# Performance work log

Hardware: AMD Instinct MI355X
Metric: run time of the kernel (lower is better)

## Reference

```python
import jax, jax.numpy as jnp
import numpy as np

B, S, D = 2, 2048, 1024
H = 16
HD = D // H

def setup_inputs() -> dict:
    key = jax.random.key(0)
    ks = jax.random.split(key, 6)
    sc = 0.02
    return {
        'x': jax.random.normal(ks[0], (B, S, D), jnp.float32),
        'Wq': jax.random.normal(ks[1], (D, D), jnp.float32) * sc,
        'Wk': jax.random.normal(ks[2], (D, D), jnp.float32) * sc,
        'Wv': jax.random.normal(ks[3], (D, D), jnp.float32) * sc,
        'Wo': jax.random.normal(ks[4], (D, D), jnp.float32) * sc,
        'bo': jnp.zeros((D,), jnp.float32),
    }

def reference(x, Wq, Wk, Wv, Wo, bo):
    b, s, d_in = x.shape
    # torch Linear: y = x @ W.T
    q = jnp.einsum('bsd,ed->bse', x, Wq)
    k = jnp.einsum('bsd,ed->bse', x, Wk)
    v = jnp.einsum('bsd,ed->bse', x, Wv)
    # [b, h, s, hd]
    q = q.reshape(b, s, H, HD).transpose(0, 2, 1, 3)
    k = k.reshape(b, s, H, HD).transpose(0, 2, 1, 3)
    v = v.reshape(b, s, H, HD).transpose(0, 2, 1, 3)
    # NOTE: original divides by sqrt(d_out), not sqrt(head_dim)
    scores = jnp.einsum('bhqd,bhkd->bhqk', q, k) / jnp.sqrt(jnp.float32(D))
    causal = jnp.tril(jnp.ones((s, s), dtype=bool))  # True = keep
    scores = jnp.where(causal[None, None], scores, -jnp.inf)
    attn = jax.nn.softmax(scores, axis=-1)
    ctx = jnp.einsum('bhqk,bhkd->bhqd', attn, v)
    ctx = ctx.transpose(0, 2, 1, 3).reshape(b, s, D)
    return jnp.einsum('bsd,ed->bse', ctx, Wo) + bo
```

## Files before the change

### kernel.cpp

```cpp
#include <hip/hip_runtime.h>
#include <hip/hip_bf16.h>
#include <stdint.h>

typedef unsigned short u16;
typedef __attribute__((ext_vector_type(8))) short short8;
typedef __attribute__((ext_vector_type(4))) float f32x4;
typedef __attribute__((ext_vector_type(16))) float f32x16;
typedef __attribute__((ext_vector_type(4))) u16 u16x4;

#define NB 2
#define NS 2048
#define ND 1024
#define NH 16
#define NM 4096

#define QSCALE 0.045084220f

#if __has_builtin(__builtin_amdgcn_exp2f)
#define EXP2(x) __builtin_amdgcn_exp2f(x)
#else
__device__ __forceinline__ float __exp2_asm(float x){
  float r;
  asm("v_exp_f32 %0, %1" : "=v"(r) : "v"(x));
  return r;
}
#define EXP2(x) __exp2_asm(x)
#endif
#if __has_builtin(__builtin_amdgcn_rcpf)
#define RCP(x) __builtin_amdgcn_rcpf(x)
#else
#define RCP(x) (1.0f / (x))
#endif

__device__ __forceinline__ u16 f2bf(float f){
  union { float f; unsigned u; } v; v.f = f;
  unsigned r = v.u + 0x7fff + ((v.u >> 16) & 1);
  return (u16)(r >> 16);
}

__device__ __forceinline__ unsigned cvtpk(float lo, float hi){
  unsigned r;
  asm("v_cvt_pk_bf16_f32 %0, %1, %2" : "=v"(r) : "v"(lo), "v"(hi));
  return r;
}

__device__ __forceinline__ void pl32swap(unsigned &e, unsigned &o){
  asm("v_permlane32_swap_b32 %0, %1" : "+v"(e), "+v"(o));
}

__device__ __forceinline__ void gload_lds16(const u16* g, u16* l){
  __builtin_amdgcn_global_load_lds(
      (const __attribute__((address_space(1))) unsigned int*)g,
      (__attribute__((address_space(3))) unsigned int*)l, 16, 0, 0);
}

__device__ __forceinline__ f32x16 mfma32(short8 a, short8 b, f32x16 c){
  return __builtin_amdgcn_mfma_f32_32x32x16_bf16(a, b, c, 0, 0, 0);
}

__global__ void cvt_kernel(const float* __restrict__ src, u16* __restrict__ dst, int n){
  int i = (blockIdx.x * blockDim.x + threadIdx.x) * 4;
  if (i < n){
    float4 v = *(const float4*)(src + i);
    u16x4 o = { f2bf(v.x), f2bf(v.y), f2bf(v.z), f2bf(v.w) };
    *(u16x4*)(dst + i) = o;
  }
}

__global__ void cvt4_kernel(const float* __restrict__ a, const float* __restrict__ b,
                            const float* __restrict__ c, const float* __restrict__ d,
                            u16* __restrict__ oa, u16* __restrict__ ob,
                            u16* __restrict__ oc, u16* __restrict__ od){
  const float* s; u16* o;
  switch (blockIdx.y){
    case 0: s = a; o = oa; break;
    case 1: s = b; o = ob; break;
    case 2: s = c; o = oc; break;
    default: s = d; o = od; break;
  }
  int i = (blockIdx.x * blockDim.x + threadIdx.x) * 4;
  float4 v = *(const float4*)(s + i);
  u16x4 pk = { f2bf(v.x), f2bf(v.y), f2bf(v.z), f2bf(v.w) };
  *(u16x4*)(o + i) = pk;
}

__device__ __forceinline__ void gemm_core(
    const u16* __restrict__ A, const u16* __restrict__ W,
    int m0, int n0, u16* lsA, u16* lsB, f32x4 acc[4][4])
{
  const int tid = threadIdx.x;
  const int l   = tid & 63;
  const int wr  = (tid >> 7) & 1;
  const int wc  = (tid >> 6) & 1;
  const int lr  = l & 15;
  const int lkb = (l >> 4) << 4;
  const int sr  = tid >> 3;
  const int scb = (tid & 7) << 4;

  for (int kt = 0; kt < 16; ++kt){
    const int k0 = kt << 6;
    #pragma unroll
    for (int i = 0; i < 4; ++i){
      int r   = (i << 5) + sr;
      int cbs = scb ^ ((r & 7) << 4);
      gload_lds16(&A[(size_t)(m0 + r) * ND + k0 + (cbs >> 1)], &lsA[r * 64 + (scb >> 1)]);
      gload_lds16(&W[(size_t)(n0 + r) * ND + k0 + (cbs >> 1)], &lsB[r * 64 + (scb >> 1)]);
    }
    __syncthreads();

    short8 af[4][2], bf[4][2];
    #pragma unroll
    for (int m16 = 0; m16 < 4; ++m16){
      int r  = (wr << 6) + (m16 << 4) + lr;
      int rx = (r & 7) << 4;
      #pragma unroll
      for (int ks = 0; ks < 2; ++ks){
        int off = r * 128 + (((ks << 6) + lkb) ^ rx);
        af[m16][ks] = *(const short8*)((const char*)lsA + off);
      }
    }
    #pragma unroll
    for (int n16 = 0; n16 < 4; ++n16){
      int r  = (wc << 6) + (n16 << 4) + lr;
      int rx = (r & 7) << 4;
      #pragma unroll
      for (int ks = 0; ks < 2; ++ks){
        int off = r * 128 + (((ks << 6) + lkb) ^ rx);
        bf[n16][ks] = *(const short8*)((const char*)lsB + off);
      }
    }
    #pragma unroll
    for (int m16 = 0; m16 < 4; ++m16)
      #pragma unroll
      for (int n16 = 0; n16 < 4; ++n16){
        acc[m16][n16] = __builtin_amdgcn_mfma_f32_16x16x32_bf16(af[m16][0], bf[n16][0], acc[m16][n16], 0, 0, 0);
        acc[m16][n16] = __builtin_amdgcn_mfma_f32_16x16x32_bf16(af[m16][1], bf[n16][1], acc[m16][n16], 0, 0, 0);
      }
    __syncthreads();
  }
}

__global__ __launch_bounds__(256) void gemm_qkv(
    const u16* __restrict__ xb,
    const u16* __restrict__ Wqb, const u16* __restrict__ Wkb, const u16* __restrict__ Wvb,
    u16* __restrict__ Qo, u16* __restrict__ Ko, u16* __restrict__ Vt)
{
  __shared__ u16 lsA[128*64];
  __shared__ u16 lsB[128*64];
  const int z = blockIdx.z;
  const u16* W = (z == 0) ? Wqb : (z == 1) ? Wkb : Wvb;
  const int m0 = blockIdx.x << 7, n0 = blockIdx.y << 7;
  f32x4 acc[4][4] = {};
  gemm_core(xb, W, m0, n0, lsA, lsB, acc);

  const int l  = threadIdx.x & 63;
  const int wr = (threadIdx.x >> 7) & 1, wc = (threadIdx.x >> 6) & 1;
  const int rb = m0 + (wr << 6) + ((l >> 4) << 2);
  const int cb = n0 + (wc << 6) + (l & 15);

  if (z < 2){
    const float sc = (z == 0) ? QSCALE : 1.0f;
    u16* C = (z == 0) ? Qo : Ko;
    #pragma unroll
    for (int m16 = 0; m16 < 4; ++m16)
      #pragma unroll
      for (int n16 = 0; n16 < 4; ++n16)
        #pragma unroll
        for (int r = 0; r < 4; ++r)
          C[(size_t)(rb + (m16 << 4) + r) * ND + cb + (n16 << 4)] = f2bf(acc[m16][n16][r] * sc);
  } else {
    #pragma unroll
    for (int m16 = 0; m16 < 4; ++m16){
      int srow = rb + (m16 << 4);
      int bi = srow >> 11, s = srow & 2047;
      #pragma unroll
      for (int n16 = 0; n16 < 4; ++n16){
        int col = cb + (n16 << 4);
        u16x4 pk = { f2bf(acc[m16][n16][0]), f2bf(acc[m16][n16][1]),
                     f2bf(acc[m16][n16][2]), f2bf(acc[m16][n16][3]) };
        *(u16x4*)&Vt[((size_t)(bi * 16 + (col >> 6)) * 64 + (col & 63)) * 2048 + s] = pk;
      }
    }
  }
}

__global__ __launch_bounds__(256) void gemm_out(
    const u16* __restrict__ ctxb, const u16* __restrict__ Wob,
    const float* __restrict__ bo, float* __restrict__ out)
{
  __shared__ u16 lsA[128*64];
  __shared__ u16 lsB[128*64];
  const int m0 = blockIdx.x << 7, n0 = blockIdx.y << 7;
  f32x4 acc[4][4] = {};
  gemm_core(ctxb, Wob, m0, n0, lsA, lsB, acc);

  const int l  = threadIdx.x & 63;
  const int wr = (threadIdx.x >> 7) & 1, wc = (threadIdx.x >> 6) & 1;
  const int rb = m0 + (wr << 6) + ((l >> 4) << 2);
  const int cb = n0 + (wc << 6) + (l & 15);
  #pragma unroll
  for (int m16 = 0; m16 < 4; ++m16)
    #pragma unroll
    for (int n16 = 0; n16 < 4; ++n16)
      #pragma unroll
      for (int r = 0; r < 4; ++r){
        int col = cb + (n16 << 4);
        out[(size_t)(rb + (m16 << 4) + r) * ND + col] = acc[m16][n16][r] + bo[col];
      }
}

__device__ __forceinline__ void stage_tile(const u16* src, int srcStride, u16* lds, int tid){
  const int rl = tid >> 3;
  const int ch = tid & 7;
  const int cs = ch ^ (rl & 7);
  gload_lds16(&src[(size_t)rl * srcStride + cs * 8],        &lds[rl * 64 + ch * 8]);
  gload_lds16(&src[(size_t)(rl + 32) * srcStride + cs * 8], &lds[(rl + 32) * 64 + ch * 8]);
}

__device__ __forceinline__ void qk_tile(const u16* lsKt, const short8 qf[4],
                                        int q5, int hi, f32x16 &s0, f32x16 &s1){
  const char* Kc = (const char*)lsKt;
  const int swz = q5 & 7;
  f32x16 a = {}, b = {};
  __builtin_amdgcn_s_setprio(1);
  #pragma unroll
  for (int ks = 0; ks < 4; ++ks){
    int c0 = ((2 * ks + hi) ^ swz) << 4;
    short8 k0 = *(const short8*)(Kc + q5 * 128 + c0);
    short8 k1 = *(const short8*)(Kc + (q5 + 32) * 128 + c0);
    a = mfma32(k0, qf[ks], a);
    b = mfma32(k1, qf[ks], b);
  }
  __builtin_amdgcn_s_setprio(0);
  s0 = a; s1 = b;
}

__device__ __forceinline__ void sm_pv(f32x16 s0, f32x16 s1, const u16* lsVt,
                                      int t, int qb, int qgl, int q5, int hi,
                                      float &m_r, float &l_r, f32x16 &accA, f32x16 &accB){
  if (t * 64 + 63 > qb){
    #pragma unroll
    for (int r = 0; r < 16; ++r){
      int kl = t * 64 + (r & 3) + 8 * (r >> 2) + 4 * hi;
      if (kl > qgl)      s0[r] = -3e38f;
      if (kl + 32 > qgl) s1[r] = -3e38f;
    }
  }
  float mx[16];
  #pragma unroll
  for (int r = 0; r < 16; ++r) mx[r] = fmaxf(s0[r], s1[r]);
  #pragma unroll
  for (int stp = 8; stp > 0; stp >>= 1)
    #pragma unroll
    for (int r = 0; r < stp; ++r) mx[r] = fmaxf(mx[r], mx[r + stp]);
  float pm = fmaxf(mx[0], __shfl_xor(mx[0], 32));

  if (__any(pm > m_r + 8.f)){
    float mn = fmaxf(m_r, pm);
    float e  = EXP2(m_r - mn);
    m_r = mn; l_r *= e;
    #pragma unroll
    for (int r = 0; r < 16; ++r){ accA[r] *= e; accB[r] *= e; }
  }

  #pragma unroll
  for (int r = 0; r < 16; ++r){
    s0[r] = EXP2(s0[r] - m_r);
    s1[r] = EXP2(s1[r] - m_r);
  }
  float sm[16];
  #pragma unroll
  for (int r = 0; r < 16; ++r) sm[r] = s0[r] + s1[r];
  #pragma unroll
  for (int stp = 8; stp > 0; stp >>= 1)
    #pragma unroll
    for (int r = 0; r < stp; ++r) sm[r] += sm[r + stp];
  l_r += sm[0] + __shfl_xor(sm[0], 32);

  unsigned pw[2][4][2];
  #pragma unroll
  for (int g = 0; g < 4; ++g){
    pw[0][g][0] = cvtpk(s0[4*g],     s0[4*g + 1]);
    pw[0][g][1] = cvtpk(s0[4*g + 2], s0[4*g + 3]);
    pw[1][g][0] = cvtpk(s1[4*g],     s1[4*g + 1]);
    pw[1][g][1] = cvtpk(s1[4*g + 2], s1[4*g + 3]);
  }
  #pragma unroll
  for (int m = 0; m < 2; ++m)
    #pragma unroll
    for (int kp = 0; kp < 2; ++kp)
      #pragma unroll
      for (int i = 0; i < 2; ++i)
        pl32swap(pw[m][2*kp][i], pw[m][2*kp + 1][i]);

  const char* Vc = (const char*)lsVt;
  const int swz = q5 & 7;
  __builtin_amdgcn_s_setprio(1);
  #pragma unroll
  for (int ks = 0; ks < 4; ++ks){
    const int m = ks >> 1, kp = ks & 1;
    union { unsigned u[4]; short8 s8; } pa;
    pa.u[0] = pw[m][2*kp][0];
    pa.u[1] = pw[m][2*kp][1];
    pa.u[2] = pw[m][2*kp + 1][0];
    pa.u[3] = pw[m][2*kp + 1][1];
    int c0 = ((2 * ks + hi) ^ swz) << 4;
    short8 v0 = *(const short8*)(Vc + q5 * 128 + c0);
    short8 v1 = *(const short8*)(Vc + (q5 + 32) * 128 + c0);
    accA = mfma32(pa.s8, v0, accA);
    accB = mfma32(pa.s8, v1, accB);
  }
  __builtin_amdgcn_s_setprio(0);
}

#define SUBITER(T, SC0, SC1, SN0, SN1)                                            \
  {                                                                               \
    const int t_ = (T);                                                           \
    if (t_ + 3 <= tb){                                                            \
      stage_tile(&Kb0[(size_t)(t_ + 3) * 64 * ND], ND, lsK[(t_ + 3) & 3], tid);   \
      stage_tile(&Vb0[(t_ + 3) * 64],              NS, lsV[(t_ + 3) & 3], tid);   \
    }                                                                             \
    if (t_ + 1 <= nc) qk_tile(lsK[(t_ + 1) & 3], qf, q5, hi, SN0, SN1);           \
    if (t_ <= nc)     sm_pv(SC0, SC1, lsV[t_ & 3], t_, qb, qgl, q5, hi,           \
                            m_r, l_r, accA, accB);                                \
    if (t_ + 3 <= tb) asm volatile("s_waitcnt vmcnt(4)" ::: "memory");            \
    else              asm volatile("s_waitcnt vmcnt(0)" ::: "memory");            \
    __builtin_amdgcn_sched_barrier(0);                                            \
    __builtin_amdgcn_s_barrier();                                                 \
    __builtin_amdgcn_sched_barrier(0);                                            \
  }

__global__ __launch_bounds__(256, 2) void attn_kernel(
    const u16* __restrict__ Q, const u16* __restrict__ K,
    const u16* __restrict__ Vt, u16* __restrict__ ctx)
{
  __shared__ __align__(16) u16 lsK[4][64*64];
  __shared__ __align__(16) u16 lsV[4][64*64];

  const int bid = blockIdx.x;
  const int xcd = bid & 7;
  const int j   = bid >> 3;
  const int strm = (j & 31) >> 3;
  const int idx  = j & 7;
  const int st   = (j < 32) ? (15 - idx) : idx;
  const int bh   = xcd + 8 * strm;
  const int b = bh >> 4, h = bh & 15;
  const int tid = threadIdx.x;
  const int l = tid & 63, w = tid >> 6;
  const int q5 = l & 31, hi = l >> 5;
  const int qb   = st * 128 + w * 32;
  const int qgl  = qb + q5;
  const int nc   = (qb + 31) >> 6;
  const int tb   = 2 * st + 1;

  const u16* Kb0 = &K[(size_t)(b * NS) * ND + h * 64];
  const u16* Vb0 = &Vt[(size_t)bh * 64 * NS];

  short8 qf[4];
  {
    const u16* Qrow = &Q[(size_t)(b * NS + qgl) * ND + h * 64 + hi * 8];
    #pragma unroll
    for (int ks = 0; ks < 4; ++ks)
      qf[ks] = *(const short8*)&Qrow[ks * 16];
  }

  float m_r = -3e38f, l_r = 0.f;
  f32x16 accA = {}, accB = {};
  f32x16 sA0, sA1, sB0, sB1;

  stage_tile(Kb0, ND, lsK[0], tid);
  stage_tile(Vb0, NS, lsV[0], tid);
  stage_tile(&Kb0[(size_t)64 * ND], ND, lsK[1], tid);
  stage_tile(&Vb0[64],              NS, lsV[1], tid);
  if (2 <= tb){
    stage_tile(&Kb0[(size_t)128 * ND], ND, lsK[2], tid);
    stage_tile(&Vb0[128],              NS, lsV[2], tid);
    asm volatile("s_waitcnt vmcnt(4)" ::: "memory");
  } else {
    asm volatile("s_waitcnt vmcnt(0)" ::: "memory");
  }
  __builtin_amdgcn_sched_barrier(0);
  __builtin_amdgcn_s_barrier();
  __builtin_amdgcn_sched_barrier(0);
  qk_tile(lsK[0], qf, q5, hi, sA0, sA1);

  #pragma unroll 1
  for (int t = 0; t <= tb; t += 2){
    SUBITER(t,     sA0, sA1, sB0, sB1);
    SUBITER(t + 1, sB0, sB1, sA0, sA1);
  }

  float inv = RCP(l_r);
  #pragma unroll
  for (int r = 0; r < 16; ++r){
    int qrow = (r & 3) + 8 * (r >> 2) + 4 * hi;
    float iv = __shfl(inv, (l & 32) | qrow, 64);
    u16* crow = &ctx[(size_t)(b * NS + qb + qrow) * ND + h * 64 + q5];
    crow[0]  = f2bf(accA[r] * iv);
    crow[32] = f2bf(accB[r] * iv);
  }
}

extern "C" void kernel_launch(void* const* d_in, const int* in_sizes, int n_in,
                              void* d_out, int out_size, void* d_ws, size_t ws_size,
                              hipStream_t stream)
{
  const float* x  = (const float*)d_in[0];
  const float* Wq = (const float*)d_in[1];
  const float* Wk = (const float*)d_in[2];
  const float* Wv = (const float*)d_in[3];
  const float* Wo = (const float*)d_in[4];
  const float* bo = (const float*)d_in[5];
  float* out = (float*)d_out;
  char* ws = (char*)d_ws;

  u16* xb  = (u16*)(ws);
  u16* Wqb = (u16*)(ws + (8u  << 20));
  u16* Wkb = (u16*)(ws + (10u << 20));
  u16* Wvb = (u16*)(ws + (12u << 20));
  u16* Wob = (u16*)(ws + (14u << 20));
  u16* Qb  = (u16*)(ws + (16u << 20));
  u16* Kb  = (u16*)(ws + (24u << 20));
  u16* Vtb = (u16*)(ws + (32u << 20));
  u16* Cb  = (u16*)(ws + (40u << 20));

  cvt_kernel<<<4096, 256, 0, stream>>>(x, xb, NM * ND);
  cvt4_kernel<<<dim3(1024, 4), 256, 0, stream>>>(Wq, Wk, Wv, Wo, Wqb, Wkb, Wvb, Wob);

  gemm_qkv<<<dim3(32, 8, 3), 256, 0, stream>>>(xb, Wqb, Wkb, Wvb, Qb, Kb, Vtb);
  attn_kernel<<<512, 256, 0, stream>>>(Qb, Kb, Vtb, Cb);
  gemm_out<<<dim3(32, 8), 256, 0, stream>>>(Cb, Wob, bo, out);
}
```

Measured before the change: 125.5 us.

## Merge conversion kernels and shrink output GEMM tile to 64 rows

The separate x and weight bf16 conversion kernels are merged into one launch, removing one kernel launch and its gap. The output projection GEMM now uses 64x128 tiles with each of four waves owning a 32-column strip, so the grid grows from 256 to 512 blocks. This is meant to fill more compute units on the device. The cost is lower reuse of the Wo tile per block and a rewritten inner loop using 16x16x32 MFMA instructions.

```diff
diff --git a/kernel.cpp b/kernel.cpp
--- a/kernel.cpp
+++ b/kernel.cpp
@@ -58,30 +58,24 @@
   return __builtin_amdgcn_mfma_f32_32x32x16_bf16(a, b, c, 0, 0, 0);
 }
 
-__global__ void cvt_kernel(const float* __restrict__ src, u16* __restrict__ dst, int n){
-  int i = (blockIdx.x * blockDim.x + threadIdx.x) * 4;
-  if (i < n){
-    float4 v = *(const float4*)(src + i);
-    u16x4 o = { f2bf(v.x), f2bf(v.y), f2bf(v.z), f2bf(v.w) };
-    *(u16x4*)(dst + i) = o;
-  }
-}
-
-__global__ void cvt4_kernel(const float* __restrict__ a, const float* __restrict__ b,
-                            const float* __restrict__ c, const float* __restrict__ d,
-                            u16* __restrict__ oa, u16* __restrict__ ob,
-                            u16* __restrict__ oc, u16* __restrict__ od){
-  const float* s; u16* o;
-  switch (blockIdx.y){
-    case 0: s = a; o = oa; break;
-    case 1: s = b; o = ob; break;
-    case 2: s = c; o = oc; break;
-    default: s = d; o = od; break;
-  }
-  int i = (blockIdx.x * blockDim.x + threadIdx.x) * 4;
+__global__ void cvt_all(const float* __restrict__ x,
+                        const float* __restrict__ wq, const float* __restrict__ wk,
+                        const float* __restrict__ wv, const float* __restrict__ wo,
+                        u16* __restrict__ xb, u16* __restrict__ wqb, u16* __restrict__ wkb,
+                        u16* __restrict__ wvb, u16* __restrict__ wob){
+  int ib = blockIdx.x;
+  const float* s; u16* d; int off;
+  if (ib < 4096){ s = x; d = xb; off = ib; }
+  else {
+    int t = ib - 4096, sel = t >> 10;
+    off = t & 1023;
+    s = (sel == 0) ? wq : (sel == 1) ? wk : (sel == 2) ? wv : wo;
+    d = (sel == 0) ? wqb : (sel == 1) ? wkb : (sel == 2) ? wvb : wob;
+  }
+  int i = (off * 256 + threadIdx.x) * 4;
   float4 v = *(const float4*)(s + i);
   u16x4 pk = { f2bf(v.x), f2bf(v.y), f2bf(v.z), f2bf(v.w) };
-  *(u16x4*)(o + i) = pk;
+  *(u16x4*)(d + i) = pk;
 }
 
 __device__ __forceinline__ void gemm_core(
@@ -188,20 +182,67 @@
     const u16* __restrict__ ctxb, const u16* __restrict__ Wob,
     const float* __restrict__ bo, float* __restrict__ out)
 {
-  __shared__ u16 lsA[128*64];
+  __shared__ u16 lsA[64*64];
   __shared__ u16 lsB[128*64];
-  const int m0 = blockIdx.x << 7, n0 = blockIdx.y << 7;
-  f32x4 acc[4][4] = {};
-  gemm_core(ctxb, Wob, m0, n0, lsA, lsB, acc);
-
-  const int l  = threadIdx.x & 63;
-  const int wr = (threadIdx.x >> 7) & 1, wc = (threadIdx.x >> 6) & 1;
-  const int rb = m0 + (wr << 6) + ((l >> 4) << 2);
-  const int cb = n0 + (wc << 6) + (l & 15);
+  const int m0 = blockIdx.x << 6, n0 = blockIdx.y << 7;
+  const int tid = threadIdx.x;
+  const int l = tid & 63;
+  const int w = tid >> 6;
+  const int lr = l & 15;
+  const int lkb = (l >> 4) << 4;
+  const int rl = tid >> 3, ch = tid & 7;
+
+  f32x4 acc[4][2] = {};
+
+  for (int kt = 0; kt < 16; ++kt){
+    const int k0 = kt << 6;
+    #pragma unroll
+    for (int k = 0; k < 2; ++k){
+      int rr = rl + (k << 5);
+      int cs = ch ^ (rr & 7);
+      gload_lds16(&ctxb[(size_t)(m0 + rr) * ND + k0 + cs * 8], &lsA[rr * 64 + ch * 8]);
+    }
+    #pragma unroll
+    for (int k = 0; k < 4; ++k){
+      int rr = rl + (k << 5);
+      int cs = ch ^ (rr & 7);
+      gload_lds16(&Wob[(size_t)(n0 + rr) * ND + k0 + cs * 8], &lsB[rr * 64 + ch * 8]);
+    }
+    __syncthreads();
+
+    short8 af[4][2], bf[2][2];
+    #pragma unroll
+    for (int m16 = 0; m16 < 4; ++m16){
+      int r  = (m16 << 4) + lr;
+      int rx = (r & 7) << 4;
+      #pragma unroll
+      for (int ks = 0; ks < 2; ++ks)
+        af[m16][ks] = *(const short8*)((const char*)lsA + r * 128 + (((ks << 6) + lkb) ^ rx));
+    }
+    #pragma unroll
+    for (int n16 = 0; n16 < 2; ++n16){
+      int r  = (w << 5) + (n16 << 4) + lr;
+      int rx = (r & 7) << 4;
+      #pragma unroll
+      for (int ks = 0; ks < 2; ++ks)
+        bf[n16][ks] = *(const short8*)((const char*)lsB + r * 128 + (((ks << 6) + lkb) ^ rx));
+    }
+    #pragma unroll
+    for (int m16 = 0; m16 < 4; ++m16)
+      #pragma unroll
+      for (int n16 = 0; n16 < 2; ++n16){
+        acc[m16][n16] = __builtin_amdgcn_mfma_f32_16x16x32_bf16(af[m16][0], bf[n16][0], acc[m16][n16], 0, 0, 0);
+        acc[m16][n16] = __builtin_amdgcn_mfma_f32_16x16x32_bf16(af[m16][1], bf[n16][1], acc[m16][n16], 0, 0, 0);
+      }
+    __syncthreads();
+  }
+
+  const int rb = m0 + ((l >> 4) << 2);
+  const int cb = n0 + (w << 5) + lr;
   #pragma unroll
   for (int m16 = 0; m16 < 4; ++m16)
     #pragma unroll
-    for (int n16 = 0; n16 < 4; ++n16)
+    for (int n16 = 0; n16 < 2; ++n16)
       #pragma unroll
       for (int r = 0; r < 4; ++r){
         int col = cb + (n16 << 4);
@@ -424,10 +465,9 @@
   u16* Vtb = (u16*)(ws + (32u << 20));
   u16* Cb  = (u16*)(ws + (40u << 20));
 
-  cvt_kernel<<<4096, 256, 0, stream>>>(x, xb, NM * ND);
-  cvt4_kernel<<<dim3(1024, 4), 256, 0, stream>>>(Wq, Wk, Wv, Wo, Wqb, Wkb, Wvb, Wob);
+  cvt_all<<<8192, 256, 0, stream>>>(x, Wq, Wk, Wv, Wo, xb, Wqb, Wkb, Wvb, Wob);
 
   gemm_qkv<<<dim3(32, 8, 3), 256, 0, stream>>>(xb, Wqb, Wkb, Wvb, Qb, Kb, Vtb);
   attn_kernel<<<512, 256, 0, stream>>>(Qb, Kb, Vtb, Cb);
-  gemm_out<<<dim3(32, 8), 256, 0, stream>>>(Cb, Wob, bo, out);
-}
+  gemm_out<<<dim3(64, 8), 256, 0, stream>>>(Cb, Wob, bo, out);
+}
```

After: 117.4 us. 1.07x faster.
